# Kernel tuning notes

Measured on AMD Instinct MI355X. Metric: run time of the kernel, lower is better.

## Reference

```python
import jax, jax.numpy as jnp
import numpy as np

ALPHA = 1000.0


def setup_inputs() -> dict:
    key = jax.random.key(0)
    ks = jax.random.split(key, 5)
    B, D_in, K = 8192, 2048, 256  # K = n_clusters = embed_dim (square cluster_reps)
    x = jax.random.normal(ks[0], (B, D_in), dtype=jnp.float32)
    W_enc = jax.random.normal(ks[1], (D_in, K), dtype=jnp.float32) * (1.0 / np.sqrt(D_in))
    b_enc = jnp.zeros((K,), dtype=jnp.float32)
    W_dec = jax.random.normal(ks[2], (K, D_in), dtype=jnp.float32) * (1.0 / np.sqrt(K))
    b_dec = jnp.zeros((D_in,), dtype=jnp.float32)
    cluster_reps = jax.random.normal(ks[3], (K, K), dtype=jnp.float32)
    return {"x": x, "W_enc": W_enc, "b_enc": b_enc, "W_dec": W_dec,
            "b_dec": b_dec, "cluster_reps": cluster_reps}


def reference(x, W_enc, b_enc, W_dec, b_dec, cluster_reps):
    # Autoencoder (linear MLP stand-in for the injected module)
    emb = x @ W_enc + b_enc                    # [B, K]
    reconstruction = emb @ W_dec + b_dec       # [B, D_in]

    # Squared Euclidean distance to each cluster rep, in GEMM form: [B, K]
    # dist[b, k] = ||emb_b||^2 - 2 emb_b . c_k + ||c_k||^2
    dist = (jnp.sum(emb * emb, axis=1, keepdims=True)
            - 2.0 * (emb @ cluster_reps.T)
            + jnp.sum(cluster_reps * cluster_reps, axis=1)[None, :])

    stack_dist = dist.T                        # [K, B] (matches torch.stack over clusters)
    min_dist = jnp.min(stack_dist, axis=0)     # [B]
    stack_exp = jnp.exp(-ALPHA * (stack_dist - min_dist[None, :]))  # stable softmin
    softmax = stack_exp / jnp.sum(stack_exp, axis=0, keepdims=True)
    weighted_dist = stack_dist * softmax       # [K, B]
    return weighted_dist, reconstruction
```

## Files before the change

kernel.cpp:

```cpp
#include <hip/hip_runtime.h>

#define ALPHA_F 1000.0f

typedef _Float16 half8 __attribute__((ext_vector_type(8)));
typedef float floatx4 __attribute__((ext_vector_type(4)));

__device__ __forceinline__ void gload_lds16(const void* g, void* l) {
    __builtin_amdgcn_global_load_lds(
        (const __attribute__((address_space(1))) unsigned int*)g,
        (__attribute__((address_space(3))) unsigned int*)l, 16, 0, 0);
}

__global__ __launch_bounds__(256) void split_wenc(
    const float* __restrict__ W, _Float16* __restrict__ Wh, _Float16* __restrict__ Wl)
{
    const int q = blockIdx.x * 256 + threadIdx.x;
    const int n = q & 255, k8 = q >> 8;
    const int k = k8 * 8;
    half8 h, l;
    #pragma unroll
    for (int i = 0; i < 8; ++i) {
        const float v = W[(size_t)(k + i) * 256 + n] * 256.0f;
        const _Float16 hi = (_Float16)v;
        h[i] = hi;
        l[i] = (_Float16)(v - (float)hi);
    }
    const int kc = k >> 5, nt = n >> 4;
    const int lane = (n & 15) | ((k8 & 3) << 4);
    const size_t idx = (size_t)((kc * 16 + nt) * 64 + lane) * 8;
    *(half8*)(Wh + idx) = h;
    *(half8*)(Wl + idx) = l;
}

__global__ __launch_bounds__(256) void split_wdec(
    const float* __restrict__ W, _Float16* __restrict__ Wh)
{
    const int q = blockIdx.x * 256 + threadIdx.x;
    const int n = q & 2047, k8 = q >> 11;
    const int k = k8 * 8;
    half8 h;
    #pragma unroll
    for (int i = 0; i < 8; ++i) h[i] = (_Float16)W[(size_t)(k + i) * 2048 + n];
    const int kc = k8 >> 2, nt = n >> 4;
    const int lane = (n & 15) | ((k8 & 3) << 4);
    *(half8*)(Wh + (size_t)((kc * 128 + nt) * 64 + lane) * 8) = h;
}

__global__ __launch_bounds__(256) void split_creps(
    const float* __restrict__ C, _Float16* __restrict__ Ch, _Float16* __restrict__ Cl)
{
    const int q = blockIdx.x * 256 + threadIdx.x;
    const int n = q & 255, j8 = q >> 8;
    const int j = j8 * 8;
    half8 h, l;
    #pragma unroll
    for (int i = 0; i < 8; ++i) {
        const float v = C[(size_t)n * 256 + j + i];
        const _Float16 hi = (_Float16)v;
        h[i] = hi;
        l[i] = (_Float16)((v - (float)hi) * 2048.0f);
    }
    const int jc = j >> 5, nt = n >> 4;
    const int lane = (n & 15) | ((j8 & 3) << 4);
    const size_t idx = (size_t)((jc * 16 + nt) * 64 + lane) * 8;
    *(half8*)(Ch + idx) = h;
    *(half8*)(Cl + idx) = l;
}

__global__ __launch_bounds__(256) void emb_gemm(
    const float* __restrict__ x, const _Float16* __restrict__ Wh,
    const _Float16* __restrict__ Wl, float* __restrict__ P)
{
    __shared__ _Float16 Ah[4 * 64 * 8], Al[4 * 64 * 8];
    __shared__ _Float16 Bh[16 * 64 * 8], Bl[16 * 64 * 8];
    const int t = threadIdx.x, lane = t & 63, w = t >> 6;
    const int kk = blockIdx.x;
    const int mb = blockIdx.y;
    const int m0 = mb * 64;

    const int am = t >> 2, q = t & 3;
    _Float16* AhW = Ah + (((am >> 4) * 64) + ((am & 15) | (q << 4))) * 8;
    _Float16* AlW = Al + (((am >> 4) * 64) + ((am & 15) | (q << 4))) * 8;
    const float* xP = x + (size_t)(m0 + am) * 2048 + kk * 256 + q * 8;

    floatx4 acc[4][4] = {};

    for (int it = 0; it < 8; ++it) {
        const float4 v0 = *(const float4*)(xP + it * 32);
        const float4 v1 = *(const float4*)(xP + it * 32 + 4);
        const int kc = kk * 8 + it;
        __syncthreads();
        const _Float16* bh_src = Wh + (size_t)kc * 16 * 512;
        const _Float16* bl_src = Wl + (size_t)kc * 16 * 512;
        #pragma unroll
        for (int i = 0; i < 4; ++i) {
            const int c = w * 4 + i;
            gload_lds16(bh_src + (size_t)c * 512 + lane * 8, Bh + c * 512);
            gload_lds16(bl_src + (size_t)c * 512 + lane * 8, Bl + c * 512);
        }
        half8 h8, l8;
        {
            const float vv[8] = {v0.x, v0.y, v0.z, v0.w, v1.x, v1.y, v1.z, v1.w};
            #pragma unroll
            for (int i = 0; i < 8; ++i) {
                const _Float16 hi = (_Float16)vv[i];
                h8[i] = hi;
                l8[i] = (_Float16)(vv[i] - (float)hi);
            }
        }
        *(half8*)AhW = h8;
        *(half8*)AlW = l8;
        __syncthreads();

        half8 ah[4], al[4], bh[4], bl[4];
        #pragma unroll
        for (int s = 0; s < 4; ++s) {
            ah[s] = *(const half8*)(Ah + (s * 64 + lane) * 8);
            al[s] = *(const half8*)(Al + (s * 64 + lane) * 8);
        }
        #pragma unroll
        for (int ni = 0; ni < 4; ++ni) {
            bh[ni] = *(const half8*)(Bh + ((w * 4 + ni) * 64 + lane) * 8);
            bl[ni] = *(const half8*)(Bl + ((w * 4 + ni) * 64 + lane) * 8);
        }
        #pragma unroll
        for (int mi = 0; mi < 4; ++mi) {
            #pragma unroll
            for (int ni = 0; ni < 4; ++ni) {
                acc[mi][ni] = __builtin_amdgcn_mfma_f32_16x16x32_f16(ah[mi], bl[ni], acc[mi][ni], 0, 0, 0);
                acc[mi][ni] = __builtin_amdgcn_mfma_f32_16x16x32_f16(al[mi], bh[ni], acc[mi][ni], 0, 0, 0);
                acc[mi][ni] = __builtin_amdgcn_mfma_f32_16x16x32_f16(ah[mi], bh[ni], acc[mi][ni], 0, 0, 0);
            }
        }
    }

    float* Pb = P + ((size_t)(kk * 128 + mb) * 16) * 1024;
    #pragma unroll
    for (int mi = 0; mi < 4; ++mi)
        #pragma unroll
        for (int ni = 0; ni < 4; ++ni)
            *(floatx4*)(Pb + (size_t)(mi * 4 + ni) * 1024 + t * 4) = acc[mi][ni];
}

__global__ __launch_bounds__(256) void finalize(
    const float* __restrict__ P, const float* __restrict__ b_enc,
    _Float16* __restrict__ eh, _Float16* __restrict__ el,
    float* __restrict__ enorm)
{
    __shared__ float femb[32 * 257];
    const int t = threadIdx.x, lane = t & 63, w = t >> 6;
    const int mb = blockIdx.x >> 1, half_ = blockIdx.x & 1;
    const int mi2 = half_ * 2;

    floatx4 acc[2][4] = {};
    #pragma unroll
    for (int kk = 0; kk < 8; ++kk) {
        const float* Pb = P + ((size_t)(kk * 128 + mb) * 16) * 1024;
        #pragma unroll
        for (int dmi = 0; dmi < 2; ++dmi)
            #pragma unroll
            for (int ni = 0; ni < 4; ++ni) {
                const floatx4 v = *(const floatx4*)(Pb + (size_t)((mi2 + dmi) * 4 + ni) * 1024 + t * 4);
                acc[dmi][ni] += v;
            }
    }

    const float inv = 1.0f / 256.0f;
    #pragma unroll
    for (int dmi = 0; dmi < 2; ++dmi) {
        #pragma unroll
        for (int ni = 0; ni < 4; ++ni) {
            const int col = w * 64 + ni * 16 + (lane & 15);
            const float bias = b_enc[col];
            const int rowL = dmi * 16 + (lane >> 4) * 4;
            #pragma unroll
            for (int r = 0; r < 4; ++r)
                femb[(rowL + r) * 257 + col] = acc[dmi][ni][r] * inv + bias;
        }
    }
    __syncthreads();

    const int rowL = t >> 3;
    float ssq = 0.0f;
    #pragma unroll
    for (int oo = 0; oo < 4; ++oo) {
        const int oid = t * 4 + oo;
        const int q = oid & 31;
        const float* src = femb + rowL * 257 + q * 8;
        half8 h, l;
        #pragma unroll
        for (int i = 0; i < 8; ++i) {
            const float v = src[i];
            const _Float16 hi = (_Float16)v;
            h[i] = hi;
            l[i] = (_Float16)((v - (float)hi) * 2048.0f);
            ssq += v * v;
        }
        const int grow = mb * 64 + half_ * 32 + rowL;
        const size_t idx = (size_t)(((grow >> 4) * 8 + (q >> 2)) * 64
                                    + ((grow & 15) | ((q & 3) << 4))) * 8;
        *(half8*)(eh + idx) = h;
        *(half8*)(el + idx) = l;
    }
    ssq += __shfl_xor(ssq, 1, 64);
    ssq += __shfl_xor(ssq, 2, 64);
    ssq += __shfl_xor(ssq, 4, 64);
    if ((t & 7) == 0) enorm[mb * 64 + half_ * 32 + rowL] = ssq;
}

__global__ __launch_bounds__(256) void recon_gemm(
    const _Float16* __restrict__ embh, const _Float16* __restrict__ Wdh,
    const float* __restrict__ b_dec, float* __restrict__ out)
{
    __shared__ _Float16 Ah[8 * 64 * 8];
    __shared__ _Float16 Bh[8 * 64 * 8];
    const int t = threadIdx.x, lane = t & 63, w = t >> 6;
    const int wm = w >> 1, wn = w & 1;
    const int nb = blockIdx.x, mb = blockIdx.y;

    floatx4 acc[4][4] = {};

    for (int kc = 0; kc < 8; ++kc) {
        __syncthreads();
        #pragma unroll
        for (int i = 0; i < 2; ++i) {
            const int c = w * 2 + i;
            gload_lds16(embh + (size_t)(((mb * 8 + c) * 8 + kc) * 64 + lane) * 8, Ah + c * 512);
            gload_lds16(Wdh + (size_t)((kc * 128 + nb * 8 + c) * 64 + lane) * 8, Bh + c * 512);
        }
        __syncthreads();
        half8 a[4], b[4];
        #pragma unroll
        for (int mi = 0; mi < 4; ++mi) a[mi] = *(const half8*)(Ah + ((wm * 4 + mi) * 64 + lane) * 8);
        #pragma unroll
        for (int ni = 0; ni < 4; ++ni) b[ni] = *(const half8*)(Bh + ((wn * 4 + ni) * 64 + lane) * 8);
        #pragma unroll
        for (int mi = 0; mi < 4; ++mi)
            #pragma unroll
            for (int ni = 0; ni < 4; ++ni)
                acc[mi][ni] = __builtin_amdgcn_mfma_f32_16x16x32_f16(a[mi], b[ni], acc[mi][ni], 0, 0, 0);
    }

    #pragma unroll
    for (int ni = 0; ni < 4; ++ni) {
        const int col = nb * 128 + (wn * 4 + ni) * 16 + (lane & 15);
        const float bias = b_dec[col];
        #pragma unroll
        for (int mi = 0; mi < 4; ++mi) {
            const int rowBase = mb * 128 + (wm * 4 + mi) * 16 + (lane >> 4) * 4;
            #pragma unroll
            for (int r = 0; r < 4; ++r)
                out[(size_t)(rowBase + r) * 2048 + col] = acc[mi][ni][r] + bias;
        }
    }
}

__global__ __launch_bounds__(256) void row_sumsq(
    const float* __restrict__ src, float* __restrict__ dst)
{
    const int wid = threadIdx.x >> 6, lane = threadIdx.x & 63;
    const int row = blockIdx.x * 4 + wid;
    const float4 v = *(const float4*)(src + (size_t)row * 256 + lane * 4);
    float s = v.x * v.x + v.y * v.y + v.z * v.z + v.w * v.w;
    #pragma unroll
    for (int off = 32; off >= 1; off >>= 1) s += __shfl_xor(s, off, 64);
    if (lane == 0) dst[row] = s;
}

__global__ __launch_bounds__(256) void dist_softmin(
    const _Float16* __restrict__ eh, const _Float16* __restrict__ el,
    const _Float16* __restrict__ ch, const _Float16* __restrict__ cl,
    const float* __restrict__ enorm, const float* __restrict__ cnorm,
    float* __restrict__ out)
{
    __shared__ float D[32 * 257];
    __shared__ float MINV[32], SUMV[32];
    const int t = threadIdx.x, lane = t & 63, w = t >> 6;
    const int b0 = blockIdx.x * 32;
    const int mt0 = blockIdx.x * 2;

    floatx4 acc[2][4] = {}, accX[2][4] = {};
    for (int kc = 0; kc < 8; ++kc) {
        half8 ah[2], al[2];
        #pragma unroll
        for (int mi = 0; mi < 2; ++mi) {
            const size_t ab = (size_t)(((mt0 + mi) * 8 + kc) * 64 + lane) * 8;
            ah[mi] = *(const half8*)(eh + ab);
            al[mi] = *(const half8*)(el + ab);
        }
        #pragma unroll
        for (int ni = 0; ni < 4; ++ni) {
            const size_t bb = (size_t)((kc * 16 + (w * 4 + ni)) * 64 + lane) * 8;
            const half8 bh = *(const half8*)(ch + bb);
            const half8 bl = *(const half8*)(cl + bb);
            #pragma unroll
            for (int mi = 0; mi < 2; ++mi) {
                acc[mi][ni]  = __builtin_amdgcn_mfma_f32_16x16x32_f16(ah[mi], bh, acc[mi][ni], 0, 0, 0);
                accX[mi][ni] = __builtin_amdgcn_mfma_f32_16x16x32_f16(ah[mi], bl, accX[mi][ni], 0, 0, 0);
                accX[mi][ni] = __builtin_amdgcn_mfma_f32_16x16x32_f16(al[mi], bh, accX[mi][ni], 0, 0, 0);
            }
        }
    }

    const float invs = 1.0f / 2048.0f;
    #pragma unroll
    for (int mi = 0; mi < 2; ++mi) {
        #pragma unroll
        for (int ni = 0; ni < 4; ++ni) {
            const int k = w * 64 + ni * 16 + (lane & 15);
            const float cn = cnorm[k];
            #pragma unroll
            for (int r = 0; r < 4; ++r) {
                const int rl = mi * 16 + (lane >> 4) * 4 + r;
                const float S = acc[mi][ni][r] + accX[mi][ni][r] * invs;
                D[rl * 257 + k] = enorm[b0 + rl] - 2.0f * S + cn;
            }
        }
    }
    __syncthreads();

    #pragma unroll
    for (int rr = 0; rr < 8; ++rr) {
        const int r = w * 8 + rr;
        const float d0 = D[r * 257 + lane +   0];
        const float d1 = D[r * 257 + lane +  64];
        const float d2 = D[r * 257 + lane + 128];
        const float d3 = D[r * 257 + lane + 192];
        float mn = fminf(fminf(d0, d1), fminf(d2, d3));
        #pragma unroll
        for (int off = 32; off >= 1; off >>= 1) mn = fminf(mn, __shfl_xor(mn, off, 64));
        float s = expf(-ALPHA_F * (d0 - mn)) + expf(-ALPHA_F * (d1 - mn))
                + expf(-ALPHA_F * (d2 - mn)) + expf(-ALPHA_F * (d3 - mn));
        #pragma unroll
        for (int off = 32; off >= 1; off >>= 1) s += __shfl_xor(s, off, 64);
        if (lane == 0) { MINV[r] = mn; SUMV[r] = s; }
    }
    __syncthreads();

    const int b = t & 31, kg = t >> 5;
    const float mn = MINV[b], sv = SUMV[b];
    #pragma unroll
    for (int kk = 0; kk < 32; ++kk) {
        const int k = kk * 8 + kg;
        const float dv = D[b * 257 + k];
        out[(size_t)k * 8192 + b0 + b] = dv * expf(-ALPHA_F * (dv - mn)) / sv;
    }
}

extern "C" void kernel_launch(void* const* d_in, const int* in_sizes, int n_in,
                              void* d_out, int out_size, void* d_ws, size_t ws_size,
                              hipStream_t stream) {
    const float* x     = (const float*)d_in[0];
    const float* W_enc = (const float*)d_in[1];
    const float* b_enc = (const float*)d_in[2];
    const float* W_dec = (const float*)d_in[3];
    const float* b_dec = (const float*)d_in[4];
    const float* creps = (const float*)d_in[5];

    float* out_w   = (float*)d_out;
    float* out_rec = out_w + (size_t)256 * 8192;
    float* P       = out_rec;

    float*     enorm = (float*)d_ws;
    float*     cnorm = enorm + 8192;
    _Float16*  embh  = (_Float16*)(cnorm + 256);
    _Float16*  embl  = embh + (size_t)8192 * 256;
    _Float16*  Whf   = embl + (size_t)8192 * 256;
    _Float16*  Wlf   = Whf + (size_t)2048 * 256;
    _Float16*  Wdh   = Wlf + (size_t)2048 * 256;
    _Float16*  crh   = Wdh + (size_t)256 * 2048;
    _Float16*  crl   = crh + (size_t)256 * 256;

    split_wenc<<<256, 256, 0, stream>>>(W_enc, Whf, Wlf);
    split_wdec<<<256, 256, 0, stream>>>(W_dec, Wdh);
    split_creps<<<32, 256, 0, stream>>>(creps, crh, crl);
    row_sumsq<<<64, 256, 0, stream>>>(creps, cnorm);

    emb_gemm<<<dim3(8, 128), 256, 0, stream>>>(x, Whf, Wlf, P);

    finalize<<<256, 256, 0, stream>>>(P, b_enc, embh, embl, enorm);

    dist_softmin<<<256, 256, 0, stream>>>(embh, embl, crh, crl, enorm, cnorm, out_w);

    recon_gemm<<<dim3(16, 64), 256, 0, stream>>>(embh, Wdh, b_dec, out_rec);
}
```

Measured before the change: 220.2 us.

## Drop LDS staging in GEMMs, load MFMA fragments directly from global memory

Both emb_gemm and recon_gemm stop staging tiles through shared memory with global_load_lds and __syncthreads. Each wave now loads its A and B fragments straight from global memory into registers, with the x split into hi/lo halves done per wave. emb_gemm also halves the split-K factor from 8 to 4, so each block covers 512 of K, and finalize reduces fewer partials. This removes barriers and LDS traffic, but every wave in emb_gemm now loads and converts the same x rows redundantly, and the grid is smaller, giving less parallelism.

Result: slower. 226.9 us (+3.0%).

```diff
diff --git a/kernel.cpp b/kernel.cpp
--- a/kernel.cpp
+++ b/kernel.cpp
@@ -4,12 +4,6 @@
 
 typedef _Float16 half8 __attribute__((ext_vector_type(8)));
 typedef float floatx4 __attribute__((ext_vector_type(4)));
-
-__device__ __forceinline__ void gload_lds16(const void* g, void* l) {
-    __builtin_amdgcn_global_load_lds(
-        (const __attribute__((address_space(1))) unsigned int*)g,
-        (__attribute__((address_space(3))) unsigned int*)l, 16, 0, 0);
-}
 
 __global__ __launch_bounds__(256) void split_wenc(
     const float* __restrict__ W, _Float16* __restrict__ Wh, _Float16* __restrict__ Wl)
@@ -71,65 +65,43 @@
     const float* __restrict__ x, const _Float16* __restrict__ Wh,
     const _Float16* __restrict__ Wl, float* __restrict__ P)
 {
-    __shared__ _Float16 Ah[4 * 64 * 8], Al[4 * 64 * 8];
-    __shared__ _Float16 Bh[16 * 64 * 8], Bl[16 * 64 * 8];
     const int t = threadIdx.x, lane = t & 63, w = t >> 6;
     const int kk = blockIdx.x;
     const int mb = blockIdx.y;
     const int m0 = mb * 64;
-
-    const int am = t >> 2, q = t & 3;
-    _Float16* AhW = Ah + (((am >> 4) * 64) + ((am & 15) | (q << 4))) * 8;
-    _Float16* AlW = Al + (((am >> 4) * 64) + ((am & 15) | (q << 4))) * 8;
-    const float* xP = x + (size_t)(m0 + am) * 2048 + kk * 256 + q * 8;
+    const int row16 = lane & 15, oct = lane >> 4;
 
     floatx4 acc[4][4] = {};
 
-    for (int it = 0; it < 8; ++it) {
-        const float4 v0 = *(const float4*)(xP + it * 32);
-        const float4 v1 = *(const float4*)(xP + it * 32 + 4);
-        const int kc = kk * 8 + it;
-        __syncthreads();
-        const _Float16* bh_src = Wh + (size_t)kc * 16 * 512;
-        const _Float16* bl_src = Wl + (size_t)kc * 16 * 512;
-        #pragma unroll
-        for (int i = 0; i < 4; ++i) {
-            const int c = w * 4 + i;
-            gload_lds16(bh_src + (size_t)c * 512 + lane * 8, Bh + c * 512);
-            gload_lds16(bl_src + (size_t)c * 512 + lane * 8, Bl + c * 512);
-        }
-        half8 h8, l8;
-        {
-            const float vv[8] = {v0.x, v0.y, v0.z, v0.w, v1.x, v1.y, v1.z, v1.w};
+    const float* xBase = x + (size_t)(m0 + row16) * 2048 + kk * 512 + oct * 8;
+
+    for (int it = 0; it < 16; ++it) {
+        half8 ah[4], al[4];
+        #pragma unroll
+        for (int mi = 0; mi < 4; ++mi) {
+            const float* p = xBase + (size_t)(mi * 16) * 2048 + it * 32;
+            const float4 u0 = *(const float4*)(p);
+            const float4 u1 = *(const float4*)(p + 4);
+            const float vv[8] = {u0.x, u0.y, u0.z, u0.w, u1.x, u1.y, u1.z, u1.w};
             #pragma unroll
             for (int i = 0; i < 8; ++i) {
                 const _Float16 hi = (_Float16)vv[i];
-                h8[i] = hi;
-                l8[i] = (_Float16)(vv[i] - (float)hi);
-            }
-        }
-        *(half8*)AhW = h8;
-        *(half8*)AlW = l8;
-        __syncthreads();
-
-        half8 ah[4], al[4], bh[4], bl[4];
-        #pragma unroll
-        for (int s = 0; s < 4; ++s) {
-            ah[s] = *(const half8*)(Ah + (s * 64 + lane) * 8);
-            al[s] = *(const half8*)(Al + (s * 64 + lane) * 8);
-        }
-        #pragma unroll
-        for (int ni = 0; ni < 4; ++ni) {
-            bh[ni] = *(const half8*)(Bh + ((w * 4 + ni) * 64 + lane) * 8);
-            bl[ni] = *(const half8*)(Bl + ((w * 4 + ni) * 64 + lane) * 8);
-        }
-        #pragma unroll
-        for (int mi = 0; mi < 4; ++mi) {
-            #pragma unroll
-            for (int ni = 0; ni < 4; ++ni) {
-                acc[mi][ni] = __builtin_amdgcn_mfma_f32_16x16x32_f16(ah[mi], bl[ni], acc[mi][ni], 0, 0, 0);
-                acc[mi][ni] = __builtin_amdgcn_mfma_f32_16x16x32_f16(al[mi], bh[ni], acc[mi][ni], 0, 0, 0);
-                acc[mi][ni] = __builtin_amdgcn_mfma_f32_16x16x32_f16(ah[mi], bh[ni], acc[mi][ni], 0, 0, 0);
+                ah[mi][i] = hi;
+                al[mi][i] = (_Float16)(vv[i] - (float)hi);
+            }
+        }
+        const int kc = kk * 16 + it;
+        const _Float16* bh_p = Wh + ((size_t)(kc * 16 + w * 4) * 64 + lane) * 8;
+        const _Float16* bl_p = Wl + ((size_t)(kc * 16 + w * 4) * 64 + lane) * 8;
+        #pragma unroll
+        for (int ni = 0; ni < 4; ++ni) {
+            const half8 bh = *(const half8*)(bh_p + (size_t)ni * 512);
+            const half8 bl = *(const half8*)(bl_p + (size_t)ni * 512);
+            #pragma unroll
+            for (int mi = 0; mi < 4; ++mi) {
+                acc[mi][ni] = __builtin_amdgcn_mfma_f32_16x16x32_f16(ah[mi], bl, acc[mi][ni], 0, 0, 0);
+                acc[mi][ni] = __builtin_amdgcn_mfma_f32_16x16x32_f16(al[mi], bh, acc[mi][ni], 0, 0, 0);
+                acc[mi][ni] = __builtin_amdgcn_mfma_f32_16x16x32_f16(ah[mi], bh, acc[mi][ni], 0, 0, 0);
             }
         }
     }
@@ -154,7 +126,7 @@
 
     floatx4 acc[2][4] = {};
     #pragma unroll
-    for (int kk = 0; kk < 8; ++kk) {
+    for (int kk = 0; kk < 4; ++kk) {
         const float* Pb = P + ((size_t)(kk * 128 + mb) * 16) * 1024;
         #pragma unroll
         for (int dmi = 0; dmi < 2; ++dmi)
@@ -212,8 +184,6 @@
     const _Float16* __restrict__ embh, const _Float16* __restrict__ Wdh,
     const float* __restrict__ b_dec, float* __restrict__ out)
 {
-    __shared__ _Float16 Ah[8 * 64 * 8];
-    __shared__ _Float16 Bh[8 * 64 * 8];
     const int t = threadIdx.x, lane = t & 63, w = t >> 6;
     const int wm = w >> 1, wn = w & 1;
     const int nb = blockIdx.x, mb = blockIdx.y;
@@ -221,24 +191,19 @@
     floatx4 acc[4][4] = {};
 
     for (int kc = 0; kc < 8; ++kc) {
-        __syncthreads();
-        #pragma unroll
-        for (int i = 0; i < 2; ++i) {
-            const int c = w * 2 + i;
-            gload_lds16(embh + (size_t)(((mb * 8 + c) * 8 + kc) * 64 + lane) * 8, Ah + c * 512);
-            gload_lds16(Wdh + (size_t)((kc * 128 + nb * 8 + c) * 64 + lane) * 8, Bh + c * 512);
-        }
-        __syncthreads();
-        half8 a[4], b[4];
-        #pragma unroll
-        for (int mi = 0; mi < 4; ++mi) a[mi] = *(const half8*)(Ah + ((wm * 4 + mi) * 64 + lane) * 8);
-        #pragma unroll
-        for (int ni = 0; ni < 4; ++ni) b[ni] = *(const half8*)(Bh + ((wn * 4 + ni) * 64 + lane) * 8);
-        #pragma unroll
-        for (int mi = 0; mi < 4; ++mi)
-            #pragma unroll
-            for (int ni = 0; ni < 4; ++ni)
-                acc[mi][ni] = __builtin_amdgcn_mfma_f32_16x16x32_f16(a[mi], b[ni], acc[mi][ni], 0, 0, 0);
+        half8 a[4];
+        #pragma unroll
+        for (int mi = 0; mi < 4; ++mi) {
+            const int mt = mb * 8 + wm * 4 + mi;
+            a[mi] = *(const half8*)(embh + (size_t)((mt * 8 + kc) * 64 + lane) * 8);
+        }
+        #pragma unroll
+        for (int ni = 0; ni < 4; ++ni) {
+            const half8 b = *(const half8*)(Wdh + (size_t)((kc * 128 + nb * 8 + wn * 4 + ni) * 64 + lane) * 8);
+            #pragma unroll
+            for (int mi = 0; mi < 4; ++mi)
+                acc[mi][ni] = __builtin_amdgcn_mfma_f32_16x16x32_f16(a[mi], b, acc[mi][ni], 0, 0, 0);
+        }
     }
 
     #pragma unroll
@@ -376,7 +341,7 @@
     split_creps<<<32, 256, 0, stream>>>(creps, crh, crl);
     row_sumsq<<<64, 256, 0, stream>>>(creps, cnorm);
 
-    emb_gemm<<<dim3(8, 128), 256, 0, stream>>>(x, Whf, Wlf, P);
+    emb_gemm<<<dim3(4, 128), 256, 0, stream>>>(x, Whf, Wlf, P);
 
     finalize<<<256, 256, 0, stream>>>(P, b_enc, embh, embl, enorm);
 
```
